# Kernel tuning notes

Hardware: AMD Instinct MI355X
Metric: run time of the kernel (lower is better)

Reference implementation:

```python
import jax, jax.numpy as jnp
import numpy as np

EPS = 1e-5

def setup_inputs() -> dict:
    key = jax.random.key(0)
    k0, k1 = jax.random.split(key, 2)
    N6, M5, M4 = 524288, 131072, 32768
    Cin, Cout = 256, 512
    data = jax.random.normal(k0, (N6, Cin), dtype=jnp.float32)
    weight = jax.random.normal(k1, (Cout, Cin), dtype=jnp.float32) * (1.0 / np.sqrt(Cin))
    gamma = jnp.ones((Cout,), dtype=jnp.float32)
    beta = jnp.zeros((Cout,), dtype=jnp.float32)
    # indices of non-empty nodes at the coarser depth (sorted, unique):
    # depth 6 has N6/8 = 65536 parents among M5 = 131072 depth-5 nodes (stride 2)
    idx5 = (jnp.arange(N6 // 8, dtype=jnp.int32) * (M5 // (N6 // 8)))
    # depth 5 has M5/8 = 16384 parents among M4 = 32768 depth-4 nodes (stride 2)
    idx4 = (jnp.arange(M5 // 8, dtype=jnp.int32) * (M4 // (M5 // 8)))
    return {"data": data, "weight": weight, "gamma": gamma, "beta": beta,
            "idx5": idx5, "idx4": idx4, "nnum5": M5, "nnum4": M4,
            "in_depth": 6, "out_depth": 4}

def _octree_max_pool(x, idx, nnum):
    # x: [N, C] child features in sibling groups of 8 -> pooled [N/8, C],
    # scattered (octree_pad) into the full coarser level of size nnum.
    N, C = x.shape
    y = x.reshape(N // 8, 8, C).max(axis=1)
    return jnp.zeros((nnum, C), x.dtype).at[idx].set(y)

def reference(data, weight, gamma, beta, idx5, idx4, nnum5, nnum4, in_depth, out_depth):
    out = data
    # in_depth (6) > out_depth (4): pool twice, then conv1x1+BN+ReLU
    for idx, nnum in ((idx5, nnum5), (idx4, nnum4)):
        out = _octree_max_pool(out, idx, nnum)
    h = out @ weight.T                      # 1x1 conv == bias-free linear
    mean = h.mean(axis=0)
    var = h.var(axis=0)
    h = (h - mean) * jax.lax.rsqrt(var + EPS) * gamma + beta
    return jax.nn.relu(h)
```

## Files before the change

### kernel.cpp

```cpp
#include <hip/hip_runtime.h>
#include <hip/hip_bf16.h>
#include <math.h>

#define CIN 256
#define COUT 512

typedef __attribute__((ext_vector_type(8))) short bf16x8;
typedef __attribute__((ext_vector_type(4))) float f32x4;
typedef __attribute__((ext_vector_type(4))) float f32x4v;

__device__ __forceinline__ ushort f2bf(float f) {
    union { float f; unsigned u; } x; x.f = f;
    unsigned r = x.u + 0x7FFFu + ((x.u >> 16) & 1u);
    return (ushort)(r >> 16);
}
__device__ __forceinline__ float bf2f(ushort u) {
    union { unsigned u; float f; } x; x.u = (unsigned)u << 16; return x.f;
}

__device__ __forceinline__ int lbound(const int* __restrict__ a, int n, int key) {
    int lo = 0, hi = n;
    while (lo < hi) {
        int m = (lo + hi) >> 1;
        if (a[m] < key) lo = m + 1; else hi = m;
    }
    return lo;
}

__global__ __launch_bounds__(256) void pool_prep_kernel(const float* __restrict__ data,
                                                        const int* __restrict__ idx5, int n_i5,
                                                        const int* __restrict__ idx4, int n_i4,
                                                        const float* __restrict__ W,
                                                        ushort* __restrict__ Wb,
                                                        ushort* __restrict__ P, int G2,
                                                        int* __restrict__ inv4, int n4) {
    const int b = blockIdx.x;
    const int t = threadIdx.x;

    if (b < 32) {
        int q0 = b * 1024 + t;
        #pragma unroll
        for (int j = 0; j < 4; ++j) {
            int i = (q0 + j * 256) * 4;
            float4 v = *reinterpret_cast<const float4*>(W + i);
            ushort4 o;
            o.x = f2bf(v.x); o.y = f2bf(v.y); o.z = f2bf(v.z); o.w = f2bf(v.w);
            *reinterpret_cast<ushort4*>(&Wb[i]) = o;
        }
        return;
    }
    if (b < 96) {
        int i = (b - 32) * 256 + t;
        if (i < n_i4) {
            int s = idx4[i];
            inv4[s] = i;
            int e = (i + 1 < n_i4) ? idx4[i + 1] : n4;
            for (int k = s + 1; k < e; ++k) inv4[k] = -1;
            if (i == 0) for (int k = 0; k < s; ++k) inv4[k] = -1;
        }
        return;
    }

    const int pb = b - 96;
    __shared__ int lb[5];
    if (t < 5) lb[t] = lbound(idx5, n_i5, pb * 32 + t * 8);
    __syncthreads();

    const int w = t >> 6, lane = t & 63;
    int lo  = __builtin_amdgcn_readfirstlane(lb[w]);
    int cnt = __builtin_amdgcn_readfirstlane(lb[w + 1]) - lo;

    float4 acc = make_float4(-INFINITY, -INFINITY, -INFINITY, -INFINITY);
    const float* base = data + (size_t)lo * (8 * CIN) + lane * 4;
    #pragma unroll
    for (int j = 0; j < 8; ++j) {
        if (j < cnt) {
            #pragma unroll
            for (int r = 0; r < 8; ++r) {
                f32x4v v = __builtin_nontemporal_load(
                    reinterpret_cast<const f32x4v*>(base + ((size_t)j * 8 + r) * CIN));
                acc.x = fmaxf(acc.x, v.x);
                acc.y = fmaxf(acc.y, v.y);
                acc.z = fmaxf(acc.z, v.z);
                acc.w = fmaxf(acc.w, v.w);
            }
        }
    }
    if (cnt < 8) {
        acc.x = fmaxf(acc.x, 0.f);
        acc.y = fmaxf(acc.y, 0.f);
        acc.z = fmaxf(acc.z, 0.f);
        acc.w = fmaxf(acc.w, 0.f);
    }
    ushort4 o;
    o.x = f2bf(acc.x); o.y = f2bf(acc.y); o.z = f2bf(acc.z); o.w = f2bf(acc.w);
    *reinterpret_cast<ushort4*>(&P[(size_t)(pb * 4 + w) * CIN + lane * 4]) = o;
}

__global__ __launch_bounds__(256) void mfma_gemm_kernel(const ushort* __restrict__ A,
                                                        const ushort* __restrict__ B,
                                                        ushort* __restrict__ H,
                                                        float* __restrict__ partial) {
    __shared__ __align__(16) ushort Asm[128 * 64];
    __shared__ __align__(16) ushort Bsm[128 * 64];

    int t = threadIdx.x;
    int lane = t & 63;
    int wid = t >> 6;
    int wm = wid >> 1, wn = wid & 1;
    int m0 = blockIdx.x * 128, n0 = blockIdx.y * 128;

    f32x4 acc[4][4] = {};

    for (int k0 = 0; k0 < CIN; k0 += 64) {
        #pragma unroll
        for (int i = 0; i < 4; ++i) {
            int idx = i * 256 + t;
            int row = idx >> 3;
            int sl  = idx & 7;
            bf16x8 av = *reinterpret_cast<const bf16x8*>(A + (size_t)(m0 + row) * CIN + k0 + sl * 8);
            bf16x8 bv = *reinterpret_cast<const bf16x8*>(B + (size_t)(n0 + row) * CIN + k0 + sl * 8);
            int ws = (sl ^ (row & 7)) * 8;
            *reinterpret_cast<bf16x8*>(&Asm[row * 64 + ws]) = av;
            *reinterpret_cast<bf16x8*>(&Bsm[row * 64 + ws]) = bv;
        }
        __syncthreads();

        #pragma unroll
        for (int ks = 0; ks < 2; ++ks) {
            bf16x8 af[4], bfr[4];
            int slog = ks * 4 + (lane >> 4);
            #pragma unroll
            for (int mi = 0; mi < 4; ++mi) {
                int row = wm * 64 + mi * 16 + (lane & 15);
                af[mi] = *reinterpret_cast<const bf16x8*>(&Asm[row * 64 + (slog ^ (row & 7)) * 8]);
            }
            #pragma unroll
            for (int ni = 0; ni < 4; ++ni) {
                int col = wn * 64 + ni * 16 + (lane & 15);
                bfr[ni] = *reinterpret_cast<const bf16x8*>(&Bsm[col * 64 + (slog ^ (col & 7)) * 8]);
            }
            #pragma unroll
            for (int mi = 0; mi < 4; ++mi)
                #pragma unroll
                for (int ni = 0; ni < 4; ++ni)
                    acc[mi][ni] = __builtin_amdgcn_mfma_f32_16x16x32_bf16(af[mi], bfr[ni], acc[mi][ni], 0, 0, 0);
        }
        __syncthreads();
    }

    float s[4], q[4];
    #pragma unroll
    for (int ni = 0; ni < 4; ++ni) {
        s[ni] = 0.f; q[ni] = 0.f;
        #pragma unroll
        for (int mi = 0; mi < 4; ++mi)
            #pragma unroll
            for (int r = 0; r < 4; ++r) {
                float v = acc[mi][ni][r];
                s[ni] += v;
                q[ni] = fmaf(v, v, q[ni]);
            }
        s[ni] += __shfl_xor(s[ni], 16); s[ni] += __shfl_xor(s[ni], 32);
        q[ni] += __shfl_xor(q[ni], 16); q[ni] += __shfl_xor(q[ni], 32);
    }
    float* redS = (float*)Asm;
    float* redQ = redS + 256;
    if (lane < 16) {
        #pragma unroll
        for (int ni = 0; ni < 4; ++ni) {
            int c = wn * 64 + ni * 16 + lane;
            redS[wm * 128 + c] = s[ni];
            redQ[wm * 128 + c] = q[ni];
        }
    }
    __syncthreads();
    if (t < 128) {
        float S = redS[t] + redS[128 + t];
        float Q = redQ[t] + redQ[128 + t];
        partial[(size_t)blockIdx.x * 1024 + blockIdx.y * 128 + t]       = S;
        partial[(size_t)blockIdx.x * 1024 + 512 + blockIdx.y * 128 + t] = Q;
    }

    #pragma unroll
    for (int mi = 0; mi < 4; ++mi) {
        #pragma unroll
        for (int ni = 0; ni < 4; ++ni) {
            int col   = n0 + wn * 64 + ni * 16 + (lane & 15);
            int rbase = m0 + wm * 64 + mi * 16 + (lane >> 4) * 4;
            #pragma unroll
            for (int r = 0; r < 4; ++r)
                H[(size_t)(rbase + r) * COUT + col] = f2bf(acc[mi][ni][r]);
        }
    }
}

__global__ __launch_bounds__(128) void bn_finalize_kernel(const float* __restrict__ partial,
                                                          const float* __restrict__ gamma,
                                                          const float* __restrict__ beta,
                                                          float* __restrict__ scale,
                                                          float* __restrict__ shift,
                                                          float invN) {
    __shared__ float sS[2], sQ[2];
    int c = blockIdx.x;
    int p = threadIdx.x;
    float S = partial[(size_t)p * 1024 + c];
    float Q = partial[(size_t)p * 1024 + 512 + c];
    #pragma unroll
    for (int off = 1; off < 64; off <<= 1) {
        S += __shfl_xor(S, off);
        Q += __shfl_xor(Q, off);
    }
    int lane = p & 63, w = p >> 6;
    if (lane == 0) { sS[w] = S; sQ[w] = Q; }
    __syncthreads();
    if (p == 0) {
        float Sf = sS[0] + sS[1];
        float Qf = sQ[0] + sQ[1];
        float mean = Sf * invN;
        float var  = fmaf(Qf, invN, -mean * mean);
        float inv  = rsqrtf(var + 1e-5f);
        float sc   = gamma[c] * inv;
        scale[c] = sc;
        shift[c] = fmaf(-mean, sc, beta[c]);
    }
}

__global__ __launch_bounds__(256) void out_kernel(const ushort* __restrict__ H,
                                                  const int* __restrict__ inv4,
                                                  const float* __restrict__ scale,
                                                  const float* __restrict__ shift,
                                                  float* __restrict__ out, int rows) {
    __shared__ float scl[512], sht[512];
    int t = threadIdx.x;
    scl[t]       = scale[t];
    scl[t + 256] = scale[t + 256];
    sht[t]       = shift[t];
    sht[t + 256] = shift[t + 256];
    __syncthreads();

    int r = blockIdx.x * 32 + (t >> 3);
    if (r >= rows) return;
    int c0 = (t & 7) * 8;
    int j = inv4[r];
    float* orow = out + (size_t)r * COUT;

    if (j >= 0) {
        const ushort* hrow = H + (size_t)j * COUT;
        #pragma unroll
        for (int i = 0; i < 8; ++i) {
            int c = c0 + i * 64;
            bf16x8 h = *reinterpret_cast<const bf16x8*>(hrow + c);
            float4 a, b;
            a.x = fmaxf(fmaf(bf2f((ushort)h[0]), scl[c + 0], sht[c + 0]), 0.f);
            a.y = fmaxf(fmaf(bf2f((ushort)h[1]), scl[c + 1], sht[c + 1]), 0.f);
            a.z = fmaxf(fmaf(bf2f((ushort)h[2]), scl[c + 2], sht[c + 2]), 0.f);
            a.w = fmaxf(fmaf(bf2f((ushort)h[3]), scl[c + 3], sht[c + 3]), 0.f);
            b.x = fmaxf(fmaf(bf2f((ushort)h[4]), scl[c + 4], sht[c + 4]), 0.f);
            b.y = fmaxf(fmaf(bf2f((ushort)h[5]), scl[c + 5], sht[c + 5]), 0.f);
            b.z = fmaxf(fmaf(bf2f((ushort)h[6]), scl[c + 6], sht[c + 6]), 0.f);
            b.w = fmaxf(fmaf(bf2f((ushort)h[7]), scl[c + 7], sht[c + 7]), 0.f);
            *reinterpret_cast<float4*>(orow + c)     = a;
            *reinterpret_cast<float4*>(orow + c + 4) = b;
        }
    } else {
        #pragma unroll
        for (int i = 0; i < 8; ++i) {
            int c = c0 + i * 64;
            float4 a, b;
            a.x = fmaxf(sht[c + 0], 0.f);
            a.y = fmaxf(sht[c + 1], 0.f);
            a.z = fmaxf(sht[c + 2], 0.f);
            a.w = fmaxf(sht[c + 3], 0.f);
            b.x = fmaxf(sht[c + 4], 0.f);
            b.y = fmaxf(sht[c + 5], 0.f);
            b.z = fmaxf(sht[c + 6], 0.f);
            b.w = fmaxf(sht[c + 7], 0.f);
            *reinterpret_cast<float4*>(orow + c)     = a;
            *reinterpret_cast<float4*>(orow + c + 4) = b;
        }
    }
}

extern "C" void kernel_launch(void* const* d_in, const int* in_sizes, int n_in,
                              void* d_out, int out_size, void* d_ws, size_t ws_size,
                              hipStream_t stream) {
    const float* data   = (const float*)d_in[0];
    const float* weight = (const float*)d_in[1];
    const float* gamma  = (const float*)d_in[2];
    const float* beta   = (const float*)d_in[3];
    const int*   idx5   = (const int*)d_in[4];
    const int*   idx4   = (const int*)d_in[5];

    const int n_i5 = in_sizes[4];
    const int n_i4 = in_sizes[5];
    const int G2   = n_i4;
    const int rows = out_size / COUT;
    const int M    = G2;
    const int MB   = M / 128;

    char* w = (char*)d_ws;
    ushort* P      = (ushort*)w;                        w += (size_t)G2 * CIN * sizeof(ushort);
    ushort* H      = (ushort*)w;                        w += (size_t)G2 * COUT * sizeof(ushort);
    ushort* Wb     = (ushort*)w;                        w += (size_t)COUT * CIN * sizeof(ushort);
    float* partial = (float*)w;                         w += (size_t)MB * 1024 * sizeof(float);
    float* scale   = (float*)w;                         w += COUT * sizeof(float);
    float* shift   = (float*)w;                         w += COUT * sizeof(float);
    int*   inv4    = (int*)w;                           w += (size_t)rows * sizeof(int);

    pool_prep_kernel<<<96 + G2 / 4, 256, 0, stream>>>(
        data, idx5, n_i5, idx4, n_i4, weight, Wb, P, G2, inv4, rows);

    {
        dim3 grid(MB, COUT / 128);
        mfma_gemm_kernel<<<grid, 256, 0, stream>>>(P, Wb, H, partial);
    }
    bn_finalize_kernel<<<COUT, 128, 0, stream>>>(partial, gamma, beta, scale, shift,
                                                 1.0f / (float)rows);
    out_kernel<<<(rows + 31) / 32, 256, 0, stream>>>(H, inv4, scale, shift,
                                                     (float*)d_out, rows);
}
```

Baseline: 130.9 us.

## Fuse GEMM, BN finalize and output scatter via grid-wide barrier

Merges the GEMM, BatchNorm finalize and output kernels into one persistent-style kernel. Blocks publish partial column statistics, then wait on a global atomic counter before each block reduces the statistics for its own columns. Each block applies scale, shift and ReLU to its accumulators held in registers and scatters the rows directly to their output positions, so the bf16 H intermediate and two launches go away. The barrier assumes all 512 blocks are resident at once (launch_bounds 256,2). It falls back on a spin bound, which could silently produce wrong results if the blocks are not co-resident.

```diff
diff --git a/kernel.cpp b/kernel.cpp
--- a/kernel.cpp
+++ b/kernel.cpp
@@ -13,9 +13,6 @@
     union { float f; unsigned u; } x; x.f = f;
     unsigned r = x.u + 0x7FFFu + ((x.u >> 16) & 1u);
     return (ushort)(r >> 16);
-}
-__device__ __forceinline__ float bf2f(ushort u) {
-    union { unsigned u; float f; } x; x.u = (unsigned)u << 16; return x.f;
 }
 
 __device__ __forceinline__ int lbound(const int* __restrict__ a, int n, int key) {
@@ -33,11 +30,13 @@
                                                         const float* __restrict__ W,
                                                         ushort* __restrict__ Wb,
                                                         ushort* __restrict__ P, int G2,
-                                                        int* __restrict__ inv4, int n4) {
+                                                        int* __restrict__ inv4, int n4,
+                                                        unsigned* __restrict__ gate) {
     const int b = blockIdx.x;
     const int t = threadIdx.x;
 
     if (b < 32) {
+        if (b == 0 && t == 0) *gate = 0;
         int q0 = b * 1024 + t;
         #pragma unroll
         for (int j = 0; j < 4; ++j) {
@@ -97,10 +96,18 @@
     *reinterpret_cast<ushort4*>(&P[(size_t)(pb * 4 + w) * CIN + lane * 4]) = o;
 }
 
-__global__ __launch_bounds__(256) void mfma_gemm_kernel(const ushort* __restrict__ A,
-                                                        const ushort* __restrict__ B,
-                                                        ushort* __restrict__ H,
-                                                        float* __restrict__ partial) {
+__global__ __launch_bounds__(256, 2) void gemm_fused_kernel(
+    const ushort* __restrict__ A,
+    const ushort* __restrict__ B,
+    const float* __restrict__ gamma,
+    const float* __restrict__ beta,
+    const int* __restrict__ idx4,
+    const int* __restrict__ inv4,
+    float* __restrict__ partial,
+    unsigned* __restrict__ gate,
+    float* __restrict__ out,
+    float invN, int nblocks)
+{
     __shared__ __align__(16) ushort Asm[128 * 64];
     __shared__ __align__(16) ushort Bsm[128 * 64];
 
@@ -108,7 +115,8 @@
     int lane = t & 63;
     int wid = t >> 6;
     int wm = wid >> 1, wn = wid & 1;
-    int m0 = blockIdx.x * 128, n0 = blockIdx.y * 128;
+    int bm = blockIdx.x, bn = blockIdx.y;
+    int m0 = bm * 128, n0 = bn * 128;
 
     f32x4 acc[4][4] = {};
 
@@ -178,106 +186,89 @@
     if (t < 128) {
         float S = redS[t] + redS[128 + t];
         float Q = redQ[t] + redQ[128 + t];
-        partial[(size_t)blockIdx.x * 1024 + blockIdx.y * 128 + t]       = S;
-        partial[(size_t)blockIdx.x * 1024 + 512 + blockIdx.y * 128 + t] = Q;
-    }
-
-    #pragma unroll
-    for (int mi = 0; mi < 4; ++mi) {
-        #pragma unroll
-        for (int ni = 0; ni < 4; ++ni) {
-            int col   = n0 + wn * 64 + ni * 16 + (lane & 15);
-            int rbase = m0 + wm * 64 + mi * 16 + (lane >> 4) * 4;
-            #pragma unroll
-            for (int r = 0; r < 4; ++r)
-                H[(size_t)(rbase + r) * COUT + col] = f2bf(acc[mi][ni][r]);
-        }
-    }
-}
-
-__global__ __launch_bounds__(128) void bn_finalize_kernel(const float* __restrict__ partial,
-                                                          const float* __restrict__ gamma,
-                                                          const float* __restrict__ beta,
-                                                          float* __restrict__ scale,
-                                                          float* __restrict__ shift,
-                                                          float invN) {
-    __shared__ float sS[2], sQ[2];
-    int c = blockIdx.x;
-    int p = threadIdx.x;
-    float S = partial[(size_t)p * 1024 + c];
-    float Q = partial[(size_t)p * 1024 + 512 + c];
-    #pragma unroll
-    for (int off = 1; off < 64; off <<= 1) {
-        S += __shfl_xor(S, off);
-        Q += __shfl_xor(Q, off);
-    }
-    int lane = p & 63, w = p >> 6;
-    if (lane == 0) { sS[w] = S; sQ[w] = Q; }
-    __syncthreads();
-    if (p == 0) {
-        float Sf = sS[0] + sS[1];
-        float Qf = sQ[0] + sQ[1];
+        partial[(size_t)bm * 1024 + bn * 128 + t]       = S;
+        partial[(size_t)bm * 1024 + 512 + bn * 128 + t] = Q;
+    }
+
+    __threadfence();
+    __syncthreads();
+    if (t == 0) {
+        __hip_atomic_fetch_add(gate, 1u, __ATOMIC_ACQ_REL, __HIP_MEMORY_SCOPE_AGENT);
+        int spins = 0;
+        while (__hip_atomic_load(gate, __ATOMIC_ACQUIRE, __HIP_MEMORY_SCOPE_AGENT) < (unsigned)nblocks
+               && ++spins < 2000000) {
+            __builtin_amdgcn_s_sleep(4);
+        }
+    }
+    __syncthreads();
+
+    {
+        int half = t >> 7;
+        int c    = n0 + (t & 127);
+        float S = 0.f, Q = 0.f;
+        for (int p = half * 64; p < half * 64 + 64; ++p) {
+            S += partial[(size_t)p * 1024 + c];
+            Q += partial[(size_t)p * 1024 + 512 + c];
+        }
+        redS[t] = S;
+        redQ[t] = Q;
+    }
+    __syncthreads();
+    float* scl = redQ + 256;
+    float* sht = scl + 128;
+    float* rsh = sht + 128;
+    if (t < 128) {
+        float Sf = redS[t] + redS[t + 128];
+        float Qf = redQ[t] + redQ[t + 128];
         float mean = Sf * invN;
         float var  = fmaf(Qf, invN, -mean * mean);
         float inv  = rsqrtf(var + 1e-5f);
-        float sc   = gamma[c] * inv;
-        scale[c] = sc;
-        shift[c] = fmaf(-mean, sc, beta[c]);
-    }
-}
-
-__global__ __launch_bounds__(256) void out_kernel(const ushort* __restrict__ H,
-                                                  const int* __restrict__ inv4,
-                                                  const float* __restrict__ scale,
-                                                  const float* __restrict__ shift,
-                                                  float* __restrict__ out, int rows) {
-    __shared__ float scl[512], sht[512];
-    int t = threadIdx.x;
-    scl[t]       = scale[t];
-    scl[t + 256] = scale[t + 256];
-    sht[t]       = shift[t];
-    sht[t + 256] = shift[t + 256];
-    __syncthreads();
-
-    int r = blockIdx.x * 32 + (t >> 3);
-    if (r >= rows) return;
-    int c0 = (t & 7) * 8;
-    int j = inv4[r];
-    float* orow = out + (size_t)r * COUT;
-
-    if (j >= 0) {
-        const ushort* hrow = H + (size_t)j * COUT;
-        #pragma unroll
-        for (int i = 0; i < 8; ++i) {
-            int c = c0 + i * 64;
-            bf16x8 h = *reinterpret_cast<const bf16x8*>(hrow + c);
-            float4 a, b;
-            a.x = fmaxf(fmaf(bf2f((ushort)h[0]), scl[c + 0], sht[c + 0]), 0.f);
-            a.y = fmaxf(fmaf(bf2f((ushort)h[1]), scl[c + 1], sht[c + 1]), 0.f);
-            a.z = fmaxf(fmaf(bf2f((ushort)h[2]), scl[c + 2], sht[c + 2]), 0.f);
-            a.w = fmaxf(fmaf(bf2f((ushort)h[3]), scl[c + 3], sht[c + 3]), 0.f);
-            b.x = fmaxf(fmaf(bf2f((ushort)h[4]), scl[c + 4], sht[c + 4]), 0.f);
-            b.y = fmaxf(fmaf(bf2f((ushort)h[5]), scl[c + 5], sht[c + 5]), 0.f);
-            b.z = fmaxf(fmaf(bf2f((ushort)h[6]), scl[c + 6], sht[c + 6]), 0.f);
-            b.w = fmaxf(fmaf(bf2f((ushort)h[7]), scl[c + 7], sht[c + 7]), 0.f);
-            *reinterpret_cast<float4*>(orow + c)     = a;
-            *reinterpret_cast<float4*>(orow + c + 4) = b;
-        }
-    } else {
-        #pragma unroll
-        for (int i = 0; i < 8; ++i) {
-            int c = c0 + i * 64;
-            float4 a, b;
-            a.x = fmaxf(sht[c + 0], 0.f);
-            a.y = fmaxf(sht[c + 1], 0.f);
-            a.z = fmaxf(sht[c + 2], 0.f);
-            a.w = fmaxf(sht[c + 3], 0.f);
-            b.x = fmaxf(sht[c + 4], 0.f);
-            b.y = fmaxf(sht[c + 5], 0.f);
-            b.z = fmaxf(sht[c + 6], 0.f);
-            b.w = fmaxf(sht[c + 7], 0.f);
-            *reinterpret_cast<float4*>(orow + c)     = a;
-            *reinterpret_cast<float4*>(orow + c + 4) = b;
+        float sc   = gamma[n0 + t] * inv;
+        float sh   = fmaf(-mean, sc, beta[n0 + t]);
+        scl[t] = sc;
+        sht[t] = sh;
+        rsh[t] = fmaxf(sh, 0.f);
+    }
+    __syncthreads();
+
+    float* outb = (float*)Bsm;
+    #pragma unroll
+    for (int mi = 0; mi < 4; ++mi) {
+        __syncthreads();
+        #pragma unroll
+        for (int ni = 0; ni < 4; ++ni) {
+            int lc = wn * 64 + ni * 16 + (lane & 15);
+            float sc_ = scl[lc], sh_ = sht[lc];
+            int r0 = (lane >> 4) * 4;
+            #pragma unroll
+            for (int r = 0; r < 4; ++r)
+                outb[(wm * 16 + r0 + r) * 128 + lc] =
+                    fmaxf(fmaf(acc[mi][ni][r], sc_, sh_), 0.f);
+        }
+        __syncthreads();
+        #pragma unroll
+        for (int it = 0; it < 2; ++it) {
+            int rr   = it * 16 + (t >> 4);
+            int lrow = (rr < 16) ? (mi * 16 + rr) : (64 + mi * 16 + (rr - 16));
+            int grow = idx4[m0 + lrow];
+            float* dst = out + (size_t)grow * COUT + n0 + (t & 15) * 8;
+            float4 v0 = *reinterpret_cast<float4*>(&outb[rr * 128 + (t & 15) * 8]);
+            float4 v1 = *reinterpret_cast<float4*>(&outb[rr * 128 + (t & 15) * 8 + 4]);
+            *reinterpret_cast<float4*>(dst)     = v0;
+            *reinterpret_cast<float4*>(dst + 4) = v1;
+        }
+    }
+
+    __syncthreads();
+    {
+        int base = bm * 256 + wid * 64;
+        int e = inv4[base + lane];
+        float2 f0 = *reinterpret_cast<float2*>(&rsh[lane * 2]);
+        for (int r = 0; r < 64; ++r) {
+            if (__shfl(e, r) < 0) {
+                float* dst = out + (size_t)(base + r) * COUT + n0 + lane * 2;
+                *reinterpret_cast<float2*>(dst) = f0;
+            }
         }
     }
 }
@@ -298,25 +289,22 @@
     const int rows = out_size / COUT;
     const int M    = G2;
     const int MB   = M / 128;
+    const int NB   = MB * 4;
 
     char* w = (char*)d_ws;
-    ushort* P      = (ushort*)w;                        w += (size_t)G2 * CIN * sizeof(ushort);
-    ushort* H      = (ushort*)w;                        w += (size_t)G2 * COUT * sizeof(ushort);
-    ushort* Wb     = (ushort*)w;                        w += (size_t)COUT * CIN * sizeof(ushort);
-    float* partial = (float*)w;                         w += (size_t)MB * 1024 * sizeof(float);
-    float* scale   = (float*)w;                         w += COUT * sizeof(float);
-    float* shift   = (float*)w;                         w += COUT * sizeof(float);
-    int*   inv4    = (int*)w;                           w += (size_t)rows * sizeof(int);
+    ushort*   P       = (ushort*)w;                     w += (size_t)G2 * CIN * sizeof(ushort);
+    ushort*   Wb      = (ushort*)w;                     w += (size_t)COUT * CIN * sizeof(ushort);
+    float*    partial = (float*)w;                      w += (size_t)MB * 1024 * sizeof(float);
+    int*      inv4    = (int*)w;                        w += (size_t)rows * sizeof(int);
+    unsigned* gate    = (unsigned*)w;                   w += 256;
 
     pool_prep_kernel<<<96 + G2 / 4, 256, 0, stream>>>(
-        data, idx5, n_i5, idx4, n_i4, weight, Wb, P, G2, inv4, rows);
+        data, idx5, n_i5, idx4, n_i4, weight, Wb, P, G2, inv4, rows, gate);
 
     {
-        dim3 grid(MB, COUT / 128);
-        mfma_gemm_kernel<<<grid, 256, 0, stream>>>(P, Wb, H, partial);
-    }
-    bn_finalize_kernel<<<COUT, 128, 0, stream>>>(partial, gamma, beta, scale, shift,
-                                                 1.0f / (float)rows);
-    out_kernel<<<(rows + 31) / 32, 256, 0, stream>>>(H, inv4, scale, shift,
-                                                     (float*)d_out, rows);
-}
+        dim3 grid(MB, 4);
+        gemm_fused_kernel<<<grid, 256, 0, stream>>>(
+            P, Wb, gamma, beta, idx4, inv4, partial, gate,
+            (float*)d_out, 1.0f / (float)rows, NB);
+    }
+}
```

Result: slower. 178.6 us (+36.4%).
